# Kernel tuning notes

Hardware: AMD Instinct MI355X
Metric: run time of the kernel (lower is better)

## Reference

```python
import jax, jax.numpy as jnp
import numpy as np

# ---- constants from init_kwargs ----
RES = 128                       # config.grid.resolution (base_resolution, n_levels=1)
LOG2_T = 22
TABLE_SIZE = 1 << LOG2_T        # hashmap entries
N_G = 4                         # features per level, gaussian grid
N_V = 8                         # features per level, vmf grid
BB_MIN = jnp.array([-10.0, -10.0, -10.0], dtype=jnp.float32)
BB_MAX = jnp.array([10.0, 10.0, 10.0], dtype=jnp.float32)
N_PTS = 1048576

_P2 = np.uint32(2654435761)
_P3 = np.uint32(805459861)
# 8 trilinear corner offsets [8,3]
_CORNERS = jnp.array([[i, j, k] for i in (0, 1) for j in (0, 1) for k in (0, 1)], dtype=jnp.int32)


def hashgrid_lookup(table, pos):
    """tcnn-style HashGrid (1 level, trilinear). pos: [N,3] in [0,1] domain."""
    x = pos * RES                     # scale to grid coords
    x0 = jnp.floor(x)
    w = x - x0                        # [N,3] trilinear weights
    corners = x0.astype(jnp.int32)[:, None, :] + _CORNERS[None]   # [N,8,3]
    cu = corners.astype(jnp.uint32)
    h = (cu[..., 0] ^ (cu[..., 1] * _P2) ^ (cu[..., 2] * _P3)) & jnp.uint32(TABLE_SIZE - 1)
    feat = table[h.astype(jnp.int32)]                              # [N,8,F] gather
    wts = jnp.prod(jnp.where(_CORNERS[None].astype(bool), w[:, None, :], 1.0 - w[:, None, :]), axis=-1)  # [N,8]
    return jnp.einsum('nc,ncf->nf', wts, feat)                     # [N,F]


def sample_vpls(pos, gauss_table, vmf_table):
    """Accumulate encodings over the 27-neighbor stencil (accumulate_gaussians=True)."""
    block = 1.0 / RES
    npos = (pos - BB_MIN) / (BB_MAX - BB_MIN)      # normalized [N,3]
    total_g = jnp.zeros((pos.shape[0], N_G), dtype=jnp.float32)
    total_v = jnp.zeros((pos.shape[0], N_V), dtype=jnp.float32)
    for dx in (-1, 0, 1):
        for dy in (-1, 0, 1):
            for dz in (-1, 0, 1):
                off = jnp.array([dx, dy, dz], dtype=jnp.float32) * block
                p = npos + off
                total_g = total_g + hashgrid_lookup(gauss_table, p)
                total_v = total_v + hashgrid_lookup(vmf_table, p)
    return total_g, total_v


def encode(gaussians, vmf):
    # gaussian_mean_encoding='sigmoid' (non-raw -> rescale to bbox)
    mean = jax.nn.sigmoid(gaussians[:, :3]) * (BB_MAX - BB_MIN) + BB_MIN
    variance = jax.nn.softplus(gaussians[:, 3])[:, None]          # 'softplus'
    sharpness = jnp.exp(vmf[:, 0])[:, None]                        # 'exp'
    ax = vmf[:, 1:4]                                               # 'normalize' (F.normalize, eps=1e-12)
    axis = ax / jnp.maximum(jnp.linalg.norm(ax, axis=1, keepdims=True), 1e-12)
    amplitude = jax.nn.sigmoid(vmf[:, 4:7])                        # 'sigmoid'
    g_out = jnp.concatenate([mean, variance], axis=1)             # [N,4]
    v_out = jnp.concatenate([sharpness, axis, amplitude], axis=1) # [N,7]
    return g_out, v_out


def setup_inputs() -> dict:
    key = jax.random.key(0)
    k1, k2, k3 = jax.random.split(key, 3)
    # world-space query positions inside the bounding box
    u = jax.random.uniform(k1, (N_PTS, 3), dtype=jnp.float32)
    pos = u * (BB_MAX - BB_MIN) + BB_MIN
    # hash-grid feature tables (tcnn initializes near zero)
    gauss_table = jax.random.normal(k2, (TABLE_SIZE, N_G), dtype=jnp.float32) * 0.1
    vmf_table = jax.random.normal(k3, (TABLE_SIZE, N_V), dtype=jnp.float32) * 0.1
    return {"pos": pos, "gauss_table": gauss_table, "vmf_table": vmf_table}


def reference(pos, gauss_table, vmf_table):
    gaussians, vmf = sample_vpls(pos, gauss_table, vmf_table)
    return encode(gaussians, vmf)
```

## Files before the change

### kernel.cpp

```cpp
#include <hip/hip_runtime.h>
#include <hip/hip_fp16.h>
#include <cstdint>

#define TABLE_MASK 0x3FFFFFu
#define P2 2654435761u
#define P3 805459861u

#define XD 128
#define YD 132
#define ZD 132
#define RECU 12
#define NB3 (128 * 128 * 8)
#define SCAN_BLKS (NB3 / 1024)

__device__ __forceinline__ float sigmoidf_(float x) { return 1.0f / (1.0f + expf(-x)); }

__device__ __forceinline__ uint32_t f2h2(float a, float b) {
    __half2 h = __floats2half2_rn(a, b);
    return *reinterpret_cast<uint32_t*>(&h);
}
__device__ __forceinline__ __half2 u2h2(uint32_t u) {
    return *reinterpret_cast<__half2*>(&u);
}

__global__ __launch_bounds__(256)
void build_exdx_kernel(const float4* __restrict__ gauss,
                       const float4* __restrict__ vmf,
                       uint32_t* __restrict__ exdx)
{
    __shared__ float sm[2][131][13];
    int bidx = blockIdx.x;
    int yp = bidx % 66;
    int rz = 1 + bidx / 66;
    int ry0 = 1 + 2 * yp;
    int t = threadIdx.x;

    for (int l = t; l < 262; l += 256) {
        int row = (l >= 131) ? 1 : 0;
        int cell = l - row * 131;
        int ry = ry0 + row;
        if (ry <= 131) {
            int xc = 1 + cell;
            uint32_t ux = (uint32_t)(xc - 2);
            uint32_t uy = (uint32_t)(ry - 2);
            uint32_t uz = (uint32_t)(rz - 2);
            uint32_t h = (ux ^ (uy * P2) ^ (uz * P3)) & TABLE_MASK;
            float4 g  = gauss[h];
            float4 v0 = vmf[(size_t)2 * h];
            float4 v1 = vmf[(size_t)2 * h + 1];
            float* s = sm[row][cell];
            s[0] = g.x;  s[1] = g.y;  s[2]  = g.z;  s[3]  = g.w;
            s[4] = v0.x; s[5] = v0.y; s[6]  = v0.z; s[7]  = v0.w;
            s[8] = v1.x; s[9] = v1.y; s[10] = v1.z; s[11] = v1.w;
        }
    }
    __syncthreads();

    int row = t >> 7;
    int c   = t & 127;
    int ry  = ry0 + row;
    if (ry > 131) return;

    uint32_t rec[12];
#pragma unroll
    for (int m = 0; m < 6; ++m) {
        float e0 = sm[row][c][2*m]   + sm[row][c+1][2*m]   + sm[row][c+2][2*m];
        float e1 = sm[row][c][2*m+1] + sm[row][c+1][2*m+1] + sm[row][c+2][2*m+1];
        float d0 = sm[row][c+3][2*m]   - sm[row][c][2*m];
        float d1 = sm[row][c+3][2*m+1] - sm[row][c][2*m+1];
        rec[m]     = f2h2(e0, e1);
        rec[6 + m] = f2h2(d0, d1);
    }
    size_t o = (((size_t)rz * YD + (size_t)ry) * XD + (size_t)c) * RECU;
    *(uint4*)(exdx + o)     = make_uint4(rec[0], rec[1], rec[2],  rec[3]);
    *(uint4*)(exdx + o + 4) = make_uint4(rec[4], rec[5], rec[6],  rec[7]);
    *(uint4*)(exdx + o + 8) = make_uint4(rec[8], rec[9], rec[10], rec[11]);
}

__device__ __forceinline__ int bin_key3(float px, float py, float pz)
{
    float x = ((px + 10.0f) / 20.0f) * 128.0f;
    float y = ((py + 10.0f) / 20.0f) * 128.0f;
    float z = ((pz + 10.0f) / 20.0f) * 128.0f;
    int ix = min(max((int)floorf(x), 0), 127);
    int iy = min(max((int)floorf(y), 0), 127);
    int iz = min(max((int)floorf(z), 0), 127);
    return (((iz << 7) + iy) << 3) + (ix >> 4);
}

__global__ __launch_bounds__(256)
void hist_kernel(const float* __restrict__ pos, uint32_t* __restrict__ hist, int n)
{
    int p = blockIdx.x * blockDim.x + threadIdx.x;
    if (p >= n) return;
    int k = bin_key3(pos[3 * p], pos[3 * p + 1], pos[3 * p + 2]);
    atomicAdd(&hist[k], 1u);
}

__global__ __launch_bounds__(1024)
void scanA_kernel(const uint32_t* __restrict__ hist,
                  uint32_t* __restrict__ cursor,
                  uint32_t* __restrict__ sums)
{
    __shared__ uint32_t buf[1024];
    int t = threadIdx.x;
    int base = blockIdx.x * 1024;
    uint32_t v = hist[base + t];
    buf[t] = v;
    __syncthreads();
    for (int off = 1; off < 1024; off <<= 1) {
        uint32_t x = (t >= off) ? buf[t - off] : 0u;
        __syncthreads();
        buf[t] += x;
        __syncthreads();
    }
    cursor[base + t] = buf[t] - v;
    if (t == 1023) sums[blockIdx.x] = buf[t];
}

__global__ __launch_bounds__(SCAN_BLKS)
void scanB_kernel(const uint32_t* __restrict__ sums, uint32_t* __restrict__ offs)
{
    __shared__ uint32_t buf[SCAN_BLKS];
    int t = threadIdx.x;
    uint32_t v = sums[t];
    buf[t] = v;
    __syncthreads();
    for (int off = 1; off < SCAN_BLKS; off <<= 1) {
        uint32_t x = (t >= off) ? buf[t - off] : 0u;
        __syncthreads();
        buf[t] += x;
        __syncthreads();
    }
    offs[t] = buf[t] - v;
}

__global__ __launch_bounds__(256)
void scatter_kernel(const float* __restrict__ pos,
                    uint32_t* __restrict__ cursor,
                    const uint32_t* __restrict__ offs,
                    float4* __restrict__ sortedPts, int n)
{
    int p = blockIdx.x * blockDim.x + threadIdx.x;
    if (p >= n) return;
    float px = pos[3 * p], py = pos[3 * p + 1], pz = pos[3 * p + 2];
    int k = bin_key3(px, py, pz);
    uint32_t slot = offs[k >> 10] + atomicAdd(&cursor[k], 1u);
    sortedPts[slot] = make_float4(px, py, pz, __uint_as_float((uint32_t)p));
}

__device__ __forceinline__ void consume_cell(const uint4& A, const uint4& B, const uint4& C,
                                             __half2 wxh, float w, float* acc)
{
    uint32_t e[6] = {A.x, A.y, A.z, A.w, B.x, B.y};
    uint32_t d[6] = {B.z, B.w, C.x, C.y, C.z, C.w};
#pragma unroll
    for (int m = 0; m < 6; ++m) {
        __half2 v = __hfma2(wxh, u2h2(d[m]), u2h2(e[m]));
        float2 f = __half22float2(v);
        acc[2*m]     = fmaf(w, f.x, acc[2*m]);
        acc[2*m + 1] = fmaf(w, f.y, acc[2*m + 1]);
    }
}

__global__ __launch_bounds__(256, 3)
void vapl_grid_sorted_kernel(const float4* __restrict__ sortedPts,
                             const uint32_t* __restrict__ exdx,
                             float* __restrict__ out,
                             int n)
{
    int bid = blockIdx.x;
    int nb  = gridDim.x;
    int b2  = ((nb & 7) == 0) ? ((bid & 7) * (nb >> 3) + (bid >> 3)) : bid;
    int s = b2 * (int)blockDim.x + (int)threadIdx.x;
    if (s >= n) return;

    float4 pt = sortedPts[s];
    int p = (int)__float_as_uint(pt.w);

    float x = ((pt.x + 10.0f) / 20.0f) * 128.0f;
    float y = ((pt.y + 10.0f) / 20.0f) * 128.0f;
    float z = ((pt.z + 10.0f) / 20.0f) * 128.0f;

    float fx = floorf(x), fy = floorf(y), fz = floorf(z);
    int ix = (int)fx, iy = (int)fy, iz = (int)fz;
    float wx = x - fx, wy = y - fy, wz = z - fz;

    float ay[4] = {1.0f - wy, 1.0f, 1.0f, wy};
    float az[4] = {1.0f - wz, 1.0f, 1.0f, wz};
    __half2 wxh = __float2half2_rn(wx);

    int bx = ix + 1, by = iy + 1, bz = iz + 1;

    uint32_t idx16[16];
    float    w16[16];
#pragma unroll
    for (int k = 0; k < 4; ++k) {
#pragma unroll
        for (int j = 0; j < 4; ++j) {
            idx16[k*4 + j] = (((uint32_t)(bz + k) * YD + (uint32_t)(by + j)) * XD
                              + (uint32_t)(bx - 1)) * RECU;
            w16[k*4 + j] = ay[j] * az[k];
        }
    }

    float acc[12] = {0.f,0.f,0.f,0.f,0.f,0.f,0.f,0.f,0.f,0.f,0.f,0.f};

    uint4 buf[2][4][3];
#pragma unroll
    for (int c = 0; c < 4; ++c) {
        const uint32_t* r = exdx + idx16[c];
        buf[0][c][0] = *(const uint4*)(r);
        buf[0][c][1] = *(const uint4*)(r + 4);
        buf[0][c][2] = *(const uint4*)(r + 8);
    }
#pragma unroll
    for (int b = 0; b < 4; ++b) {
        const int cur = b & 1, nxt = cur ^ 1;
        if (b < 3) {
#pragma unroll
            for (int c = 0; c < 4; ++c) {
                const uint32_t* r = exdx + idx16[(b + 1) * 4 + c];
                buf[nxt][c][0] = *(const uint4*)(r);
                buf[nxt][c][1] = *(const uint4*)(r + 4);
                buf[nxt][c][2] = *(const uint4*)(r + 8);
            }
        }
#pragma unroll
        for (int c = 0; c < 4; ++c) {
            consume_cell(buf[cur][c][0], buf[cur][c][1], buf[cur][c][2],
                         wxh, w16[b*4 + c], acc);
        }
    }

    float m0 = sigmoidf_(acc[0]) * 20.0f - 10.0f;
    float m1 = sigmoidf_(acc[1]) * 20.0f - 10.0f;
    float m2 = sigmoidf_(acc[2]) * 20.0f - 10.0f;
    float var = fmaxf(acc[3], 0.0f) + log1pf(expf(-fabsf(acc[3])));

    float sharp = expf(acc[4]);
    float nrm = fmaxf(sqrtf(acc[5]*acc[5] + acc[6]*acc[6] + acc[7]*acc[7]), 1e-12f);
    float a0 = acc[5] / nrm, a1 = acc[6] / nrm, a2 = acc[7] / nrm;
    float amp0 = sigmoidf_(acc[8]);
    float amp1 = sigmoidf_(acc[9]);
    float amp2 = sigmoidf_(acc[10]);

    float* og = out + (size_t)p * 4;
    *(float4*)og = make_float4(m0, m1, m2, var);

    float* ov = out + (size_t)n * 4 + (size_t)p * 7;
    ov[0] = sharp;
    ov[1] = a0;
    ov[2] = a1;
    ov[3] = a2;
    ov[4] = amp0;
    ov[5] = amp1;
    ov[6] = amp2;
}

__global__ __launch_bounds__(256)
void vapl_grid_kernel(const float* __restrict__ pos,
                      const float4* __restrict__ gauss,
                      const float4* __restrict__ vmf,
                      float* __restrict__ out,
                      int n)
{
    int p = blockIdx.x * blockDim.x + threadIdx.x;
    if (p >= n) return;

    float px = pos[3 * p + 0];
    float py = pos[3 * p + 1];
    float pz = pos[3 * p + 2];

    float x = ((px + 10.0f) / 20.0f) * 128.0f;
    float y = ((py + 10.0f) / 20.0f) * 128.0f;
    float z = ((pz + 10.0f) / 20.0f) * 128.0f;

    float fx = floorf(x), fy = floorf(y), fz = floorf(z);
    int ix = (int)fx, iy = (int)fy, iz = (int)fz;
    float wx = x - fx, wy = y - fy, wz = z - fz;

    float ax[4] = {1.0f - wx, 1.0f, 1.0f, wx};
    float ay[4] = {1.0f - wy, 1.0f, 1.0f, wy};
    float az[4] = {1.0f - wz, 1.0f, 1.0f, wz};

    uint32_t hx[4], hy[4], hz[4];
#pragma unroll
    for (int i = 0; i < 4; ++i) {
        hx[i] = (uint32_t)(ix - 1 + i);
        hy[i] = (uint32_t)(iy - 1 + i) * P2;
        hz[i] = (uint32_t)(iz - 1 + i) * P3;
    }

    float tg0 = 0.f, tg1 = 0.f, tg2 = 0.f, tg3 = 0.f;
    float tv0 = 0.f, tv1 = 0.f, tv2 = 0.f, tv3 = 0.f;
    float tv4 = 0.f, tv5 = 0.f, tv6 = 0.f, tv7 = 0.f;

    for (int k = 0; k < 4; ++k) {
        for (int j = 0; j < 4; ++j) {
            uint32_t hyz = hy[j] ^ hz[k];
            float wyz = ay[j] * az[k];
#pragma unroll
            for (int i = 0; i < 4; ++i) {
                uint32_t h = (hx[i] ^ hyz) & TABLE_MASK;
                float w = ax[i] * wyz;
                float4 g  = gauss[h];
                float4 v0 = vmf[(size_t)2 * h];
                float4 v1 = vmf[(size_t)2 * h + 1];
                tg0 = fmaf(w, g.x,  tg0);
                tg1 = fmaf(w, g.y,  tg1);
                tg2 = fmaf(w, g.z,  tg2);
                tg3 = fmaf(w, g.w,  tg3);
                tv0 = fmaf(w, v0.x, tv0);
                tv1 = fmaf(w, v0.y, tv1);
                tv2 = fmaf(w, v0.z, tv2);
                tv3 = fmaf(w, v0.w, tv3);
                tv4 = fmaf(w, v1.x, tv4);
                tv5 = fmaf(w, v1.y, tv5);
                tv6 = fmaf(w, v1.z, tv6);
                tv7 = fmaf(w, v1.w, tv7);
            }
        }
    }

    float m0 = sigmoidf_(tg0) * 20.0f - 10.0f;
    float m1 = sigmoidf_(tg1) * 20.0f - 10.0f;
    float m2 = sigmoidf_(tg2) * 20.0f - 10.0f;
    float var = fmaxf(tg3, 0.0f) + log1pf(expf(-fabsf(tg3)));

    float sharp = expf(tv0);
    float nrm = fmaxf(sqrtf(tv1 * tv1 + tv2 * tv2 + tv3 * tv3), 1e-12f);
    float a0 = tv1 / nrm, a1 = tv2 / nrm, a2 = tv3 / nrm;
    float amp0 = sigmoidf_(tv4);
    float amp1 = sigmoidf_(tv5);
    float amp2 = sigmoidf_(tv6);

    float* og = out + (size_t)p * 4;
    og[0] = m0;
    og[1] = m1;
    og[2] = m2;
    og[3] = var;

    float* ov = out + (size_t)n * 4 + (size_t)p * 7;
    ov[0] = sharp;
    ov[1] = a0;
    ov[2] = a1;
    ov[3] = a2;
    ov[4] = amp0;
    ov[5] = amp1;
    ov[6] = amp2;
}

extern "C" void kernel_launch(void* const* d_in, const int* in_sizes, int n_in,
                              void* d_out, int out_size, void* d_ws, size_t ws_size,
                              hipStream_t stream) {
    const float*  pos   = (const float*)d_in[0];
    const float4* gauss = (const float4*)d_in[1];
    const float4* vmf   = (const float4*)d_in[2];
    float* out = (float*)d_out;
    int n = in_sizes[0] / 3;

    size_t off = 0;
    char* ws = (char*)d_ws;
    uint32_t* exdx   = (uint32_t*)(ws + off);  off += (size_t)XD * YD * ZD * RECU * 4;
    off = (off + 255) & ~(size_t)255;
    uint32_t* hist   = (uint32_t*)(ws + off);  off += (size_t)NB3 * 4;
    uint32_t* cursor = (uint32_t*)(ws + off);  off += (size_t)NB3 * 4;
    uint32_t* sums   = (uint32_t*)(ws + off);  off += 256 * 4;
    uint32_t* offs   = (uint32_t*)(ws + off);  off += 256 * 4;
    off = (off + 255) & ~(size_t)255;
    float4* sortedPts = (float4*)(ws + off);   off += (size_t)n * 16;
    const size_t need = off;

    dim3 block(256);
    dim3 grid((n + 255) / 256);

    if (ws_size >= need) {
        dim3 bgrid(131 * 66);
        hipLaunchKernelGGL(build_exdx_kernel, bgrid, block, 0, stream, gauss, vmf, exdx);
        hipMemsetAsync(hist, 0, (size_t)NB3 * 4, stream);
        hipLaunchKernelGGL(hist_kernel, grid, block, 0, stream, pos, hist, n);
        hipLaunchKernelGGL(scanA_kernel, dim3(SCAN_BLKS), dim3(1024), 0, stream, hist, cursor, sums);
        hipLaunchKernelGGL(scanB_kernel, dim3(1), dim3(SCAN_BLKS), 0, stream, sums, offs);
        hipLaunchKernelGGL(scatter_kernel, grid, block, 0, stream, pos, cursor, offs, sortedPts, n);
        hipLaunchKernelGGL(vapl_grid_sorted_kernel, grid, block, 0, stream,
                           sortedPts, exdx, out, n);
    } else {
        hipLaunchKernelGGL(vapl_grid_kernel, grid, block, 0, stream, pos, gauss, vmf, out, n);
    }
}
```

Baseline: 267.1 us.

## Precompute 2D x/y box-sum and difference records per column; bin points by xy

The precomputed table now folds both the x and y stencil sums and differences into per-(x,y,z) records laid out with z fastest. Each point reads 4 z-slices of 6 uint4 in one contiguous run instead of 16 scattered cell records. Points are now binned by (y,x) column only, so neighbouring threads read adjacent z records. This cuts gather count and random accesses per point. In exchange the table grows to 24 words per cell, more math runs in fp16 (half-precision box sums), and launch bounds drop to 2 blocks per SM for the larger register footprint.

```diff
diff --git a/kernel.cpp b/kernel.cpp
--- a/kernel.cpp
+++ b/kernel.cpp
@@ -6,12 +6,9 @@
 #define P2 2654435761u
 #define P3 805459861u
 
-#define XD 128
-#define YD 132
-#define ZD 132
-#define RECU 12
-#define NB3 (128 * 128 * 8)
-#define SCAN_BLKS (NB3 / 1024)
+#define ZE 132
+#define NB2 16384
+#define SCAN2 16
 
 __device__ __forceinline__ float sigmoidf_(float x) { return 1.0f / (1.0f + expf(-x)); }
 
@@ -22,70 +19,88 @@
 __device__ __forceinline__ __half2 u2h2(uint32_t u) {
     return *reinterpret_cast<__half2*>(&u);
 }
-
-__global__ __launch_bounds__(256)
-void build_exdx_kernel(const float4* __restrict__ gauss,
+__device__ __forceinline__ uint32_t h2u(__half2 h) {
+    return *reinterpret_cast<uint32_t*>(&h);
+}
+
+__global__ __launch_bounds__(256, 4)
+void build_exdy_kernel(const float4* __restrict__ gauss,
                        const float4* __restrict__ vmf,
-                       uint32_t* __restrict__ exdx)
-{
-    __shared__ float sm[2][131][13];
-    int bidx = blockIdx.x;
-    int yp = bidx % 66;
-    int rz = 1 + bidx / 66;
-    int ry0 = 1 + 2 * yp;
+                       uint32_t* __restrict__ exdy)
+{
+    __shared__ uint32_t Rt[35][35][6];
+    int blk  = blockIdx.x;
+    int wp   = blk % ZE;
+    int tile = blk / ZE;
+    int ix0 = (tile & 3) * 32;
+    int iy0 = (tile >> 2) * 32;
+    uint32_t w = (uint32_t)(wp - 1);
     int t = threadIdx.x;
 
-    for (int l = t; l < 262; l += 256) {
-        int row = (l >= 131) ? 1 : 0;
-        int cell = l - row * 131;
-        int ry = ry0 + row;
-        if (ry <= 131) {
-            int xc = 1 + cell;
-            uint32_t ux = (uint32_t)(xc - 2);
-            uint32_t uy = (uint32_t)(ry - 2);
-            uint32_t uz = (uint32_t)(rz - 2);
-            uint32_t h = (ux ^ (uy * P2) ^ (uz * P3)) & TABLE_MASK;
-            float4 g  = gauss[h];
-            float4 v0 = vmf[(size_t)2 * h];
-            float4 v1 = vmf[(size_t)2 * h + 1];
-            float* s = sm[row][cell];
-            s[0] = g.x;  s[1] = g.y;  s[2]  = g.z;  s[3]  = g.w;
-            s[4] = v0.x; s[5] = v0.y; s[6]  = v0.z; s[7]  = v0.w;
-            s[8] = v1.x; s[9] = v1.y; s[10] = v1.z; s[11] = v1.w;
+    float4 G[5], V0[5], V1[5];
+    int ls[5];
+#pragma unroll
+    for (int it = 0; it < 5; ++it) {
+        int l = t + it * 256;
+        ls[it] = (l < 1225) ? l : -1;
+        if (ls[it] >= 0) {
+            int lu = l % 35, lv = l / 35;
+            uint32_t u = (uint32_t)(ix0 - 1 + lu);
+            uint32_t v = (uint32_t)(iy0 - 1 + lv);
+            uint32_t h = (u ^ (v * P2) ^ (w * P3)) & TABLE_MASK;
+            G[it]  = gauss[h];
+            V0[it] = vmf[(size_t)2 * h];
+            V1[it] = vmf[(size_t)2 * h + 1];
         }
     }
+#pragma unroll
+    for (int it = 0; it < 5; ++it) if (ls[it] >= 0) {
+        int lu = ls[it] % 35, lv = ls[it] / 35;
+        uint32_t* c = Rt[lv][lu];
+        c[0] = f2h2(G[it].x,  G[it].y);
+        c[1] = f2h2(G[it].z,  G[it].w);
+        c[2] = f2h2(V0[it].x, V0[it].y);
+        c[3] = f2h2(V0[it].z, V0[it].w);
+        c[4] = f2h2(V1[it].x, V1[it].y);
+        c[5] = f2h2(V1[it].z, V1[it].w);
+    }
     __syncthreads();
 
-    int row = t >> 7;
-    int c   = t & 127;
-    int ry  = ry0 + row;
-    if (ry > 131) return;
-
-    uint32_t rec[12];
-#pragma unroll
-    for (int m = 0; m < 6; ++m) {
-        float e0 = sm[row][c][2*m]   + sm[row][c+1][2*m]   + sm[row][c+2][2*m];
-        float e1 = sm[row][c][2*m+1] + sm[row][c+1][2*m+1] + sm[row][c+2][2*m+1];
-        float d0 = sm[row][c+3][2*m]   - sm[row][c][2*m];
-        float d1 = sm[row][c+3][2*m+1] - sm[row][c][2*m+1];
-        rec[m]     = f2h2(e0, e1);
-        rec[6 + m] = f2h2(d0, d1);
-    }
-    size_t o = (((size_t)rz * YD + (size_t)ry) * XD + (size_t)c) * RECU;
-    *(uint4*)(exdx + o)     = make_uint4(rec[0], rec[1], rec[2],  rec[3]);
-    *(uint4*)(exdx + o + 4) = make_uint4(rec[4], rec[5], rec[6],  rec[7]);
-    *(uint4*)(exdx + o + 8) = make_uint4(rec[8], rec[9], rec[10], rec[11]);
-}
-
-__device__ __forceinline__ int bin_key3(float px, float py, float pz)
+#pragma unroll
+    for (int oi = 0; oi < 4; ++oi) {
+        int o  = t + oi * 256;
+        int lx = o & 31, ly = o >> 5;
+        int ix = ix0 + lx, iy = iy0 + ly;
+        size_t ri = ((size_t)iy * 128 + (size_t)ix) * ZE + (size_t)wp;
+        uint32_t* dst = exdy + ri * 24;
+#pragma unroll
+        for (int m = 0; m < 6; ++m) {
+            __half2 EX[4], DX[4];
+#pragma unroll
+            for (int r = 0; r < 4; ++r) {
+                __half2 r0 = u2h2(Rt[ly + r][lx    ][m]);
+                __half2 r1 = u2h2(Rt[ly + r][lx + 1][m]);
+                __half2 r2 = u2h2(Rt[ly + r][lx + 2][m]);
+                __half2 r3 = u2h2(Rt[ly + r][lx + 3][m]);
+                EX[r] = __hadd2(__hadd2(r0, r1), r2);
+                DX[r] = __hsub2(r3, r0);
+            }
+            __half2 SEX = __hadd2(__hadd2(EX[0], EX[1]), EX[2]);
+            __half2 dEX = __hsub2(EX[3], EX[0]);
+            __half2 SDX = __hadd2(__hadd2(DX[0], DX[1]), DX[2]);
+            __half2 dDX = __hsub2(DX[3], DX[0]);
+            *(uint4*)(dst + m * 4) = make_uint4(h2u(SEX), h2u(dEX), h2u(SDX), h2u(dDX));
+        }
+    }
+}
+
+__device__ __forceinline__ int bin_key2(float px, float py)
 {
     float x = ((px + 10.0f) / 20.0f) * 128.0f;
     float y = ((py + 10.0f) / 20.0f) * 128.0f;
-    float z = ((pz + 10.0f) / 20.0f) * 128.0f;
     int ix = min(max((int)floorf(x), 0), 127);
     int iy = min(max((int)floorf(y), 0), 127);
-    int iz = min(max((int)floorf(z), 0), 127);
-    return (((iz << 7) + iy) << 3) + (ix >> 4);
+    return iy * 128 + ix;
 }
 
 __global__ __launch_bounds__(256)
@@ -93,8 +108,7 @@
 {
     int p = blockIdx.x * blockDim.x + threadIdx.x;
     if (p >= n) return;
-    int k = bin_key3(pos[3 * p], pos[3 * p + 1], pos[3 * p + 2]);
-    atomicAdd(&hist[k], 1u);
+    atomicAdd(&hist[bin_key2(pos[3 * p], pos[3 * p + 1])], 1u);
 }
 
 __global__ __launch_bounds__(1024)
@@ -118,15 +132,15 @@
     if (t == 1023) sums[blockIdx.x] = buf[t];
 }
 
-__global__ __launch_bounds__(SCAN_BLKS)
+__global__ __launch_bounds__(SCAN2)
 void scanB_kernel(const uint32_t* __restrict__ sums, uint32_t* __restrict__ offs)
 {
-    __shared__ uint32_t buf[SCAN_BLKS];
+    __shared__ uint32_t buf[SCAN2];
     int t = threadIdx.x;
     uint32_t v = sums[t];
     buf[t] = v;
     __syncthreads();
-    for (int off = 1; off < SCAN_BLKS; off <<= 1) {
+    for (int off = 1; off < SCAN2; off <<= 1) {
         uint32_t x = (t >= off) ? buf[t - off] : 0u;
         __syncthreads();
         buf[t] += x;
@@ -144,28 +158,14 @@
     int p = blockIdx.x * blockDim.x + threadIdx.x;
     if (p >= n) return;
     float px = pos[3 * p], py = pos[3 * p + 1], pz = pos[3 * p + 2];
-    int k = bin_key3(px, py, pz);
+    int k = bin_key2(px, py);
     uint32_t slot = offs[k >> 10] + atomicAdd(&cursor[k], 1u);
     sortedPts[slot] = make_float4(px, py, pz, __uint_as_float((uint32_t)p));
 }
 
-__device__ __forceinline__ void consume_cell(const uint4& A, const uint4& B, const uint4& C,
-                                             __half2 wxh, float w, float* acc)
-{
-    uint32_t e[6] = {A.x, A.y, A.z, A.w, B.x, B.y};
-    uint32_t d[6] = {B.z, B.w, C.x, C.y, C.z, C.w};
-#pragma unroll
-    for (int m = 0; m < 6; ++m) {
-        __half2 v = __hfma2(wxh, u2h2(d[m]), u2h2(e[m]));
-        float2 f = __half22float2(v);
-        acc[2*m]     = fmaf(w, f.x, acc[2*m]);
-        acc[2*m + 1] = fmaf(w, f.y, acc[2*m + 1]);
-    }
-}
-
-__global__ __launch_bounds__(256, 3)
+__global__ __launch_bounds__(256, 2)
 void vapl_grid_sorted_kernel(const float4* __restrict__ sortedPts,
-                             const uint32_t* __restrict__ exdx,
+                             const uint32_t* __restrict__ exdy,
                              float* __restrict__ out,
                              int n)
 {
@@ -186,50 +186,29 @@
     int ix = (int)fx, iy = (int)fy, iz = (int)fz;
     float wx = x - fx, wy = y - fy, wz = z - fz;
 
-    float ay[4] = {1.0f - wy, 1.0f, 1.0f, wy};
     float az[4] = {1.0f - wz, 1.0f, 1.0f, wz};
-    __half2 wxh = __float2half2_rn(wx);
-
-    int bx = ix + 1, by = iy + 1, bz = iz + 1;
-
-    uint32_t idx16[16];
-    float    w16[16];
+    __half2 wx2 = __float2half2_rn(wx);
+    __half2 wy2 = __float2half2_rn(wy);
+
+    size_t ri = ((size_t)iy * 128 + (size_t)ix) * ZE + (size_t)iz;
+    const uint4* q = (const uint4*)(exdy + ri * 24);
+    uint4 r[24];
+#pragma unroll
+    for (int j = 0; j < 24; ++j) r[j] = q[j];
+
+    float acc[12] = {0.f,0.f,0.f,0.f,0.f,0.f,0.f,0.f,0.f,0.f,0.f,0.f};
 #pragma unroll
     for (int k = 0; k < 4; ++k) {
-#pragma unroll
-        for (int j = 0; j < 4; ++j) {
-            idx16[k*4 + j] = (((uint32_t)(bz + k) * YD + (uint32_t)(by + j)) * XD
-                              + (uint32_t)(bx - 1)) * RECU;
-            w16[k*4 + j] = ay[j] * az[k];
-        }
-    }
-
-    float acc[12] = {0.f,0.f,0.f,0.f,0.f,0.f,0.f,0.f,0.f,0.f,0.f,0.f};
-
-    uint4 buf[2][4][3];
-#pragma unroll
-    for (int c = 0; c < 4; ++c) {
-        const uint32_t* r = exdx + idx16[c];
-        buf[0][c][0] = *(const uint4*)(r);
-        buf[0][c][1] = *(const uint4*)(r + 4);
-        buf[0][c][2] = *(const uint4*)(r + 8);
-    }
-#pragma unroll
-    for (int b = 0; b < 4; ++b) {
-        const int cur = b & 1, nxt = cur ^ 1;
-        if (b < 3) {
-#pragma unroll
-            for (int c = 0; c < 4; ++c) {
-                const uint32_t* r = exdx + idx16[(b + 1) * 4 + c];
-                buf[nxt][c][0] = *(const uint4*)(r);
-                buf[nxt][c][1] = *(const uint4*)(r + 4);
-                buf[nxt][c][2] = *(const uint4*)(r + 8);
-            }
-        }
-#pragma unroll
-        for (int c = 0; c < 4; ++c) {
-            consume_cell(buf[cur][c][0], buf[cur][c][1], buf[cur][c][2],
-                         wxh, w16[b*4 + c], acc);
+        float azk = az[k];
+#pragma unroll
+        for (int m = 0; m < 6; ++m) {
+            uint4 u4 = r[k * 6 + m];
+            __half2 t1 = __hfma2(wy2, u2h2(u4.y), u2h2(u4.x));
+            __half2 t2 = __hfma2(wy2, u2h2(u4.w), u2h2(u4.z));
+            __half2 tv = __hfma2(wx2, t2, t1);
+            float2 f = __half22float2(tv);
+            acc[2*m]     = fmaf(azk, f.x, acc[2*m]);
+            acc[2*m + 1] = fmaf(azk, f.y, acc[2*m + 1]);
         }
     }
 
@@ -362,12 +341,13 @@
 
     size_t off = 0;
     char* ws = (char*)d_ws;
-    uint32_t* exdx   = (uint32_t*)(ws + off);  off += (size_t)XD * YD * ZD * RECU * 4;
+    const size_t exdy_uints = (size_t)128 * 128 * ZE * 24;
+    uint32_t* exdy   = (uint32_t*)(ws + off);  off += exdy_uints * 4;
     off = (off + 255) & ~(size_t)255;
-    uint32_t* hist   = (uint32_t*)(ws + off);  off += (size_t)NB3 * 4;
-    uint32_t* cursor = (uint32_t*)(ws + off);  off += (size_t)NB3 * 4;
-    uint32_t* sums   = (uint32_t*)(ws + off);  off += 256 * 4;
-    uint32_t* offs   = (uint32_t*)(ws + off);  off += 256 * 4;
+    uint32_t* hist   = (uint32_t*)(ws + off);  off += (size_t)NB2 * 4;
+    uint32_t* cursor = (uint32_t*)(ws + off);  off += (size_t)NB2 * 4;
+    uint32_t* sums   = (uint32_t*)(ws + off);  off += 64 * 4;
+    uint32_t* offs   = (uint32_t*)(ws + off);  off += 64 * 4;
     off = (off + 255) & ~(size_t)255;
     float4* sortedPts = (float4*)(ws + off);   off += (size_t)n * 16;
     const size_t need = off;
@@ -376,15 +356,14 @@
     dim3 grid((n + 255) / 256);
 
     if (ws_size >= need) {
-        dim3 bgrid(131 * 66);
-        hipLaunchKernelGGL(build_exdx_kernel, bgrid, block, 0, stream, gauss, vmf, exdx);
-        hipMemsetAsync(hist, 0, (size_t)NB3 * 4, stream);
+        hipLaunchKernelGGL(build_exdy_kernel, dim3(16 * ZE), block, 0, stream, gauss, vmf, exdy);
+        hipMemsetAsync(hist, 0, (size_t)NB2 * 4, stream);
         hipLaunchKernelGGL(hist_kernel, grid, block, 0, stream, pos, hist, n);
-        hipLaunchKernelGGL(scanA_kernel, dim3(SCAN_BLKS), dim3(1024), 0, stream, hist, cursor, sums);
-        hipLaunchKernelGGL(scanB_kernel, dim3(1), dim3(SCAN_BLKS), 0, stream, sums, offs);
+        hipLaunchKernelGGL(scanA_kernel, dim3(SCAN2), dim3(1024), 0, stream, hist, cursor, sums);
+        hipLaunchKernelGGL(scanB_kernel, dim3(1), dim3(SCAN2), 0, stream, sums, offs);
         hipLaunchKernelGGL(scatter_kernel, grid, block, 0, stream, pos, cursor, offs, sortedPts, n);
         hipLaunchKernelGGL(vapl_grid_sorted_kernel, grid, block, 0, stream,
-                           sortedPts, exdx, out, n);
+                           sortedPts, exdy, out, n);
     } else {
         hipLaunchKernelGGL(vapl_grid_kernel, grid, block, 0, stream, pos, gauss, vmf, out, n);
     }
```

New measurement: 348.7 us. 1.31x slower.

## Merge build and histogram kernels, fold block-sum scan into scatter, deepen gather prefetch

Applied to the files above, without the earlier changes.

Runs the exdx table build and the point histogram as a single launch, with extra blocks handling the histogram. It removes the separate scanB kernel by having every scatter block redo the 256-entry exclusive scan of chunk sums in shared memory. In the main gather kernel, all 16 cell records are issued as loads before any are consumed, instead of a double-buffered four-at-a-time pipeline. Occupancy is lowered to 2 blocks per SM to make room for the extra registers. This trades fewer launches and more memory-level parallelism for redundant scan work per block and lower occupancy.

```diff
diff --git a/kernel.cpp b/kernel.cpp
--- a/kernel.cpp
+++ b/kernel.cpp
@@ -12,6 +12,7 @@
 #define RECU 12
 #define NB3 (128 * 128 * 8)
 #define SCAN_BLKS (NB3 / 1024)
+#define BUILD_BLKS (131 * 66)
 
 __device__ __forceinline__ float sigmoidf_(float x) { return 1.0f / (1.0f + expf(-x)); }
 
@@ -23,11 +24,33 @@
     return *reinterpret_cast<__half2*>(&u);
 }
 
+__device__ __forceinline__ int bin_key3(float px, float py, float pz)
+{
+    float x = ((px + 10.0f) / 20.0f) * 128.0f;
+    float y = ((py + 10.0f) / 20.0f) * 128.0f;
+    float z = ((pz + 10.0f) / 20.0f) * 128.0f;
+    int ix = min(max((int)floorf(x), 0), 127);
+    int iy = min(max((int)floorf(y), 0), 127);
+    int iz = min(max((int)floorf(z), 0), 127);
+    return (((iz << 7) + iy) << 3) + (ix >> 4);
+}
+
 __global__ __launch_bounds__(256)
-void build_exdx_kernel(const float4* __restrict__ gauss,
+void build_hist_kernel(const float4* __restrict__ gauss,
                        const float4* __restrict__ vmf,
-                       uint32_t* __restrict__ exdx)
-{
+                       uint32_t* __restrict__ exdx,
+                       const float* __restrict__ pos,
+                       uint32_t* __restrict__ hist, int n)
+{
+    if (blockIdx.x >= BUILD_BLKS) {
+        int p = (blockIdx.x - BUILD_BLKS) * blockDim.x + threadIdx.x;
+        if (p < n) {
+            int k = bin_key3(pos[3 * p], pos[3 * p + 1], pos[3 * p + 2]);
+            atomicAdd(&hist[k], 1u);
+        }
+        return;
+    }
+
     __shared__ float sm[2][131][13];
     int bidx = blockIdx.x;
     int yp = bidx % 66;
@@ -77,26 +100,6 @@
     *(uint4*)(exdx + o + 8) = make_uint4(rec[8], rec[9], rec[10], rec[11]);
 }
 
-__device__ __forceinline__ int bin_key3(float px, float py, float pz)
-{
-    float x = ((px + 10.0f) / 20.0f) * 128.0f;
-    float y = ((py + 10.0f) / 20.0f) * 128.0f;
-    float z = ((pz + 10.0f) / 20.0f) * 128.0f;
-    int ix = min(max((int)floorf(x), 0), 127);
-    int iy = min(max((int)floorf(y), 0), 127);
-    int iz = min(max((int)floorf(z), 0), 127);
-    return (((iz << 7) + iy) << 3) + (ix >> 4);
-}
-
-__global__ __launch_bounds__(256)
-void hist_kernel(const float* __restrict__ pos, uint32_t* __restrict__ hist, int n)
-{
-    int p = blockIdx.x * blockDim.x + threadIdx.x;
-    if (p >= n) return;
-    int k = bin_key3(pos[3 * p], pos[3 * p + 1], pos[3 * p + 2]);
-    atomicAdd(&hist[k], 1u);
-}
-
 __global__ __launch_bounds__(1024)
 void scanA_kernel(const uint32_t* __restrict__ hist,
                   uint32_t* __restrict__ cursor,
@@ -118,34 +121,31 @@
     if (t == 1023) sums[blockIdx.x] = buf[t];
 }
 
-__global__ __launch_bounds__(SCAN_BLKS)
-void scanB_kernel(const uint32_t* __restrict__ sums, uint32_t* __restrict__ offs)
-{
-    __shared__ uint32_t buf[SCAN_BLKS];
-    int t = threadIdx.x;
-    uint32_t v = sums[t];
-    buf[t] = v;
-    __syncthreads();
-    for (int off = 1; off < SCAN_BLKS; off <<= 1) {
-        uint32_t x = (t >= off) ? buf[t - off] : 0u;
-        __syncthreads();
-        buf[t] += x;
-        __syncthreads();
-    }
-    offs[t] = buf[t] - v;
-}
-
 __global__ __launch_bounds__(256)
 void scatter_kernel(const float* __restrict__ pos,
                     uint32_t* __restrict__ cursor,
-                    const uint32_t* __restrict__ offs,
+                    const uint32_t* __restrict__ sums,
                     float4* __restrict__ sortedPts, int n)
 {
-    int p = blockIdx.x * blockDim.x + threadIdx.x;
+    __shared__ uint32_t soff[SCAN_BLKS];
+    int t = threadIdx.x;
+    if (t < SCAN_BLKS) soff[t] = sums[t];
+    __syncthreads();
+    for (int off = 1; off < SCAN_BLKS; off <<= 1) {
+        uint32_t v = 0;
+        if (t < SCAN_BLKS && t >= off) v = soff[t - off];
+        __syncthreads();
+        if (t < SCAN_BLKS) soff[t] += v;
+        __syncthreads();
+    }
+
+    int p = blockIdx.x * blockDim.x + t;
     if (p >= n) return;
     float px = pos[3 * p], py = pos[3 * p + 1], pz = pos[3 * p + 2];
     int k = bin_key3(px, py, pz);
-    uint32_t slot = offs[k >> 10] + atomicAdd(&cursor[k], 1u);
+    int chunk = k >> 10;
+    uint32_t base = (chunk > 0) ? soff[chunk - 1] : 0u;
+    uint32_t slot = base + atomicAdd(&cursor[k], 1u);
     sortedPts[slot] = make_float4(px, py, pz, __uint_as_float((uint32_t)p));
 }
 
@@ -163,7 +163,7 @@
     }
 }
 
-__global__ __launch_bounds__(256, 3)
+__global__ __launch_bounds__(256, 2)
 void vapl_grid_sorted_kernel(const float4* __restrict__ sortedPts,
                              const uint32_t* __restrict__ exdx,
                              float* __restrict__ out,
@@ -206,32 +206,27 @@
 
     float acc[12] = {0.f,0.f,0.f,0.f,0.f,0.f,0.f,0.f,0.f,0.f,0.f,0.f};
 
-    uint4 buf[2][4][3];
-#pragma unroll
-    for (int c = 0; c < 4; ++c) {
+    uint4 A[8][3], B[8][3];
+#pragma unroll
+    for (int c = 0; c < 8; ++c) {
         const uint32_t* r = exdx + idx16[c];
-        buf[0][c][0] = *(const uint4*)(r);
-        buf[0][c][1] = *(const uint4*)(r + 4);
-        buf[0][c][2] = *(const uint4*)(r + 8);
-    }
-#pragma unroll
-    for (int b = 0; b < 4; ++b) {
-        const int cur = b & 1, nxt = cur ^ 1;
-        if (b < 3) {
-#pragma unroll
-            for (int c = 0; c < 4; ++c) {
-                const uint32_t* r = exdx + idx16[(b + 1) * 4 + c];
-                buf[nxt][c][0] = *(const uint4*)(r);
-                buf[nxt][c][1] = *(const uint4*)(r + 4);
-                buf[nxt][c][2] = *(const uint4*)(r + 8);
-            }
-        }
-#pragma unroll
-        for (int c = 0; c < 4; ++c) {
-            consume_cell(buf[cur][c][0], buf[cur][c][1], buf[cur][c][2],
-                         wxh, w16[b*4 + c], acc);
-        }
-    }
+        A[c][0] = *(const uint4*)(r);
+        A[c][1] = *(const uint4*)(r + 4);
+        A[c][2] = *(const uint4*)(r + 8);
+    }
+#pragma unroll
+    for (int c = 0; c < 8; ++c) {
+        const uint32_t* r = exdx + idx16[8 + c];
+        B[c][0] = *(const uint4*)(r);
+        B[c][1] = *(const uint4*)(r + 4);
+        B[c][2] = *(const uint4*)(r + 8);
+    }
+#pragma unroll
+    for (int c = 0; c < 8; ++c)
+        consume_cell(A[c][0], A[c][1], A[c][2], wxh, w16[c], acc);
+#pragma unroll
+    for (int c = 0; c < 8; ++c)
+        consume_cell(B[c][0], B[c][1], B[c][2], wxh, w16[8 + c], acc);
 
     float m0 = sigmoidf_(acc[0]) * 20.0f - 10.0f;
     float m1 = sigmoidf_(acc[1]) * 20.0f - 10.0f;
@@ -367,7 +362,6 @@
     uint32_t* hist   = (uint32_t*)(ws + off);  off += (size_t)NB3 * 4;
     uint32_t* cursor = (uint32_t*)(ws + off);  off += (size_t)NB3 * 4;
     uint32_t* sums   = (uint32_t*)(ws + off);  off += 256 * 4;
-    uint32_t* offs   = (uint32_t*)(ws + off);  off += 256 * 4;
     off = (off + 255) & ~(size_t)255;
     float4* sortedPts = (float4*)(ws + off);   off += (size_t)n * 16;
     const size_t need = off;
@@ -376,13 +370,11 @@
     dim3 grid((n + 255) / 256);
 
     if (ws_size >= need) {
-        dim3 bgrid(131 * 66);
-        hipLaunchKernelGGL(build_exdx_kernel, bgrid, block, 0, stream, gauss, vmf, exdx);
         hipMemsetAsync(hist, 0, (size_t)NB3 * 4, stream);
-        hipLaunchKernelGGL(hist_kernel, grid, block, 0, stream, pos, hist, n);
+        hipLaunchKernelGGL(build_hist_kernel, dim3(BUILD_BLKS + 4096), block, 0, stream,
+                           gauss, vmf, exdx, pos, hist, n);
         hipLaunchKernelGGL(scanA_kernel, dim3(SCAN_BLKS), dim3(1024), 0, stream, hist, cursor, sums);
-        hipLaunchKernelGGL(scanB_kernel, dim3(1), dim3(SCAN_BLKS), 0, stream, sums, offs);
-        hipLaunchKernelGGL(scatter_kernel, grid, block, 0, stream, pos, cursor, offs, sortedPts, n);
+        hipLaunchKernelGGL(scatter_kernel, grid, block, 0, stream, pos, cursor, sums, sortedPts, n);
         hipLaunchKernelGGL(vapl_grid_sorted_kernel, grid, block, 0, stream,
                            sortedPts, exdx, out, n);
     } else {
```

Measured after the change: 260.5 us. 1.03x faster.
